# Kernel optimization log

Measured on AMD Instinct MI355X. Metric: run time of the kernel, lower is better.

Reference implementation:

```python
import jax, jax.numpy as jnp
import numpy as np
from jax import lax

DIM, HEADS, POOL = 512, 8, 16
HD = DIM // HEADS
SCALE = HD ** -0.5


def _cbs(x, w, s, b, d=1, g=1):
    """Conv2d(bias=False, pad=d*(k-1)//2) + folded BN (scale,bias) + SiLU."""
    k = w.shape[-1]
    p = d * (k - 1) // 2
    y = lax.conv_general_dilated(x, w, (1, 1), [(p, p), (p, p)],
                                 rhs_dilation=(d, d), feature_group_count=g,
                                 dimension_numbers=("NCHW", "OIHW", "NCHW"))
    y = y * s[None, :, None, None] + b[None, :, None, None]
    return y * jax.nn.sigmoid(y)  # SiLU


def _forward(x, w01, s01, b01, w02, s02, b02, w03, s03, b03,
             w12, s12, b12, w13, s13, b13, w22, s22, b22, w23, s23, b23,
             w3, s3, b3, wkv, skv, bkv, wfc1, bfc1, wfc2, bfc2):
    bsz, c, h, w = x.shape
    # ---- _MutilScal ----
    a01 = _cbs(x, w01, s01, b01)                       # [b,128,h,w]
    a03 = _cbs(_cbs(a01, w02, s02, b02, d=3, g=128), w03, s03, b03)
    a13 = _cbs(_cbs(a01, w12, s12, b12, d=5, g=128), w13, s13, b13)
    a23 = _cbs(_cbs(a01, w22, s22, b22, d=7, g=128), w23, s23, b23)
    attn = _cbs(a03 + a13 + a23, w3, s3, b3) * x       # [b,512,h,w]
    # AdaptiveAvgPool2d(POOL): exact block mean since h,w divisible by POOL
    pooled = attn.reshape(bsz, c, POOL, h // POOL, POOL, w // POOL).mean(axis=(3, 5))
    kv = _cbs(pooled, wkv, skv, bkv)                   # [b,1024,16,16]
    # ---- pooled cross-attention ----
    n, n1 = h * w, POOL * POOL
    q = x.reshape(bsz, HEADS, HD, n).transpose(0, 1, 3, 2)          # [b,H,n,d]
    kvr = kv.reshape(bsz, 2, HEADS, HD, n1)
    k = kvr[:, 0].transpose(0, 1, 3, 2)                              # [b,H,n1,d]
    v = kvr[:, 1].transpose(0, 1, 3, 2)                              # [b,H,n1,d]
    dots = jnp.einsum("bhnd,bhmd->bhnm", q, k) * SCALE
    a = jax.nn.softmax(dots, axis=-1)
    o = jnp.einsum("bhnm,bhmd->bhnd", a, v)                          # [b,H,n,d]
    attn_out = o.transpose(0, 1, 3, 2).reshape(bsz, c, h, w)
    # ---- SE channel gate ----
    gap = x.mean(axis=(2, 3))                                        # [b,c]
    y = jnp.clip(gap @ wfc1[:, :, 0, 0].T + bfc1, 0.0, 6.0)          # ReLU6
    gate = jax.nn.sigmoid(y @ wfc2[:, :, 0, 0].T + bfc2)             # [b,c]
    c_attn = gate[:, :, None, None] * x
    return attn_out + c_attn


def setup_inputs() -> dict:
    key = jax.random.key(0)
    ks = jax.random.split(key, 32)
    ki = iter(ks)
    f = jnp.float32

    def rn(shape, scale=0.05):
        return (jax.random.normal(next(ki), shape, dtype=f) * scale)

    inp = {"x": jax.random.normal(next(ki), (8, DIM, 64, 64), dtype=f)}
    inp.update(w01=rn((128, 512, 1, 1)), s01=jnp.ones((128,), f), b01=rn((128,)))
    inp.update(w02=rn((128, 1, 3, 3)), s02=jnp.ones((128,), f), b02=rn((128,)))
    inp.update(w03=rn((512, 128, 1, 1)), s03=jnp.ones((512,), f), b03=rn((512,)))
    inp.update(w12=rn((128, 1, 3, 3)), s12=jnp.ones((128,), f), b12=rn((128,)))
    inp.update(w13=rn((512, 128, 1, 1)), s13=jnp.ones((512,), f), b13=rn((512,)))
    inp.update(w22=rn((128, 1, 3, 3)), s22=jnp.ones((128,), f), b22=rn((128,)))
    inp.update(w23=rn((512, 128, 1, 1)), s23=jnp.ones((512,), f), b23=rn((512,)))
    inp.update(w3=rn((512, 512, 1, 1)), s3=jnp.ones((512,), f), b3=rn((512,)))
    inp.update(wkv=rn((1024, 512, 1, 1)), skv=jnp.ones((1024,), f), bkv=rn((1024,)))
    inp.update(wfc1=rn((128, 512, 1, 1)), bfc1=rn((128,)))
    inp.update(wfc2=rn((512, 128, 1, 1)), bfc2=rn((512,)))
    return inp


def reference(x, w01, s01, b01, w02, s02, b02, w03, s03, b03,
              w12, s12, b12, w13, s13, b13, w22, s22, b22, w23, s23, b23,
              w3, s3, b3, wkv, skv, bkv, wfc1, bfc1, wfc2, bfc2):
    return _forward(x, w01, s01, b01, w02, s02, b02, w03, s03, b03,
                    w12, s12, b12, w13, s13, b13, w22, s22, b22, w23, s23, b23,
                    w3, s3, b3, wkv, skv, bkv, wfc1, bfc1, wfc2, bfc2)
```

## Files before the change

### kernel.cpp

```cpp
#include <hip/hip_runtime.h>
#include <cstddef>


static __device__ __forceinline__ float silu_f(float v) {
  return v / (1.f + __expf(-v));
}

typedef __attribute__((ext_vector_type(8))) short short8v;
typedef __attribute__((ext_vector_type(4))) float f32x4;

union FragU { unsigned u[4]; short8v v; uint4 q; };

#define VM_WAIT(N) asm volatile("s_waitcnt vmcnt(" #N ")" ::: "memory")
#define SBAR()     asm volatile("s_barrier" ::: "memory")

static __device__ __forceinline__ unsigned short f2bf(float f) {
  unsigned u = __builtin_bit_cast(unsigned, f);
  u += 0x7fffu + ((u >> 16) & 1u);
  return (unsigned short)(u >> 16);
}
static __device__ __forceinline__ unsigned packbf(float lo, float hi) {
  return (unsigned)f2bf(lo) | ((unsigned)f2bf(hi) << 16);
}
static __device__ __forceinline__ float bf_lo(unsigned w) {
  return __builtin_bit_cast(float, w << 16);
}
static __device__ __forceinline__ float bf_hi(unsigned w) {
  return __builtin_bit_cast(float, w & 0xffff0000u);
}

static __device__ __forceinline__ void gload16(const unsigned* gsrc, unsigned* ldst) {
  __builtin_amdgcn_global_load_lds(
      (const __attribute__((address_space(1))) unsigned*)gsrc,
      (__attribute__((address_space(3))) unsigned*)ldst, 16, 0, 0);
}

static __device__ __forceinline__ void stage_tile_g(const unsigned* __restrict__ src,
                                                    unsigned* dst, int tid) {
  gload16(src + 4 * tid, dst + 4 * tid);
  gload16(src + 4 * (tid + 512), dst + 4 * (tid + 512));
}

static __device__ __forceinline__ short8v load_frag4(const unsigned* P, int ksg, int pos) {
  FragU f;
  f.q = *(const uint4*)(P + (((ksg << 7) + pos) << 2));
  return f.v;
}

static __device__ __forceinline__ void xload16(const float* __restrict__ src, int ld,
                                               int tid, float v[16]) {
  const int pos = tid & 127, kg = tid >> 7;
  const float* p = src + pos + (size_t)(kg * 16) * ld;
#pragma unroll
  for (int i = 0; i < 16; ++i) v[i] = p[(size_t)i * ld];
}
static __device__ __forceinline__ void xload16_sum2(const float* __restrict__ a,
                                                    const float* __restrict__ b2, int ld,
                                                    int tid, float v[16]) {
  const int pos = tid & 127, kg = tid >> 7;
  const float* pA = a + pos + (size_t)(kg * 16) * ld;
  const float* pB = b2 + pos + (size_t)(kg * 16) * ld;
#pragma unroll
  for (int i = 0; i < 16; ++i) v[i] = pA[(size_t)i * ld] + pB[(size_t)i * ld];
}
static __device__ __forceinline__ void xwrite16(const float v[16], unsigned* Xp, int tid) {
  const int pos = tid & 127, kg = tid >> 7;
#pragma unroll
  for (int i2 = 0; i2 < 4; ++i2) {
    const int kq = kg * 4 + i2;
    const int r4 = (kq & 3) + ((kq >> 3) << 2);
    const int sub = (kq >> 2) & 1;
    uint2 wv;
    wv.x = packbf(v[i2 * 4 + 0], v[i2 * 4 + 1]);
    wv.y = packbf(v[i2 * 4 + 2], v[i2 * 4 + 3]);
    *(uint2*)(Xp + (((r4 << 7) + pos) << 2) + sub * 2) = wv;
  }
}
static __device__ __forceinline__ void xstore_pairs(const float v[16],
                                                    unsigned* __restrict__ Xg_bst,
                                                    int p0, int tid) {
  const int pos = tid & 127, kg = tid >> 7;
#pragma unroll
  for (int m = 0; m < 8; ++m)
    Xg_bst[(size_t)(kg * 8 + m) * 4096 + p0 + pos] = packbf(v[2 * m], v[2 * m + 1]);
}

static __device__ __forceinline__ void stage_x_pack(const float* __restrict__ src, int ld,
                                                    unsigned* Xp, int tid) {
  float v[16];
  xload16(src, ld, tid, v);
  xwrite16(v, Xp, tid);
}

#define GEMM_IDS                                            \
  const int tid = threadIdx.x;                              \
  const int w = tid >> 6, lane = tid & 63;                  \
  const int g = lane >> 4, nl = lane & 15;                  \
  const int wr = w >> 1, wc = w & 1;

#define GEMM_KSTEP_B(ACC, XB, WB)                                                  \
  _Pragma("unroll")                                                                \
  for (int ks = 0; ks < 2; ++ks) {                                                 \
    const short8v a0 = load_frag4(WB, ks * 4 + g, wr * 32 + nl);                   \
    const short8v a1 = load_frag4(WB, ks * 4 + g, wr * 32 + 16 + nl);              \
    _Pragma("unroll")                                                              \
    for (int jj = 0; jj < 4; ++jj) {                                               \
      const short8v bfr = load_frag4(XB, ks * 4 + g, wc * 64 + jj * 16 + nl);      \
      ACC[0][jj] = __builtin_amdgcn_mfma_f32_16x16x32_bf16(a0, bfr, ACC[0][jj], 0, 0, 0); \
      ACC[1][jj] = __builtin_amdgcn_mfma_f32_16x16x32_bf16(a1, bfr, ACC[1][jj], 0, 0, 0); \
    }                                                                              \
  }

__global__ __launch_bounds__(256)
void prepack_w_kernel(const float* __restrict__ w01, const float* __restrict__ w03,
                      const float* __restrict__ w13, const float* __restrict__ w23,
                      const float* __restrict__ w3, const float* __restrict__ wkv,
                      unsigned* __restrict__ img)
{
  const int t = blockIdx.x;
  const float* W; int K; int tile; unsigned* base;
  if (t < 8)       { W = w01; K = 512; tile = t;      base = img; }
  else if (t < 16) { W = w03; K = 128; tile = t - 8;  base = img + 32768; }
  else if (t < 24) { W = w13; K = 128; tile = t - 16; base = img + 65536; }
  else if (t < 32) { W = w23; K = 128; tile = t - 24; base = img + 98304; }
  else if (t < 64) { W = w3;  K = 512; tile = t - 32; base = img + 131072; }
  else             { W = wkv; K = 512; tile = t - 64; base = img + 262144; }
  const int nk = K >> 6;
  const int to = tile / nk, tk = tile - to * nk;
  unsigned* dst = base + (size_t)tile * 4096;
  for (int wi = threadIdx.x; wi < 4096; wi += 256) {
    const int r4 = wi >> 9, pos = (wi >> 2) & 127, sub = (wi >> 1) & 1, j = wi & 1;
    const int kq = (r4 & 3) + sub * 4 + ((r4 >> 2) << 3);
    const int k = tk * 64 + 4 * kq + 2 * j;
    const int oc = to * 128 + pos;
    dst[wi] = packbf(W[(size_t)oc * K + k], W[(size_t)oc * K + k + 1]);
  }
}

__global__ __launch_bounds__(512)
void gemm_a01_kernel(const float* __restrict__ X, const unsigned* __restrict__ Wimg,
                     const float* __restrict__ sc, const float* __restrict__ bi,
                     unsigned* __restrict__ A01p, unsigned* __restrict__ Ximg2)
{
  const int b = blockIdx.z, p0 = blockIdx.x * 128;
  GEMM_IDS
  __shared__ unsigned Xp[2][4096], Wp[2][4096];
  const float* Xbase = X + (size_t)b * 512 * 4096 + p0;
  unsigned* Xg_b = Ximg2 + (size_t)b * 256 * 4096;

  f32x4 acc[2][4];
#pragma unroll
  for (int i = 0; i < 2; ++i)
#pragma unroll
    for (int jj = 0; jj < 4; ++jj) acc[i][jj] = (f32x4){0.f, 0.f, 0.f, 0.f};

  {
    float vx[16];
    xload16(Xbase, 4096, tid, vx);
    stage_tile_g(Wimg, Wp[0], tid);
    xwrite16(vx, Xp[0], tid);
    xstore_pairs(vx, Xg_b, p0, tid);
  }
  __syncthreads();

  for (int st = 0; st < 8; ++st) {
    const int cur = st & 1;
    float vn[16];
    if (st < 7) {
      xload16(Xbase + (size_t)((st + 1) * 64) * 4096, 4096, tid, vn);
      stage_tile_g(Wimg + (size_t)(st + 1) * 4096, Wp[cur ^ 1], tid);
    }
    GEMM_KSTEP_B(acc, Xp[cur], Wp[cur])
    if (st < 7) {
      xwrite16(vn, Xp[cur ^ 1], tid);
      xstore_pairs(vn, Xg_b + (size_t)(32 * (st + 1)) * 4096, p0, tid);
    }
    __syncthreads();
  }

#pragma unroll
  for (int i = 0; i < 2; ++i) {
    const int base = wr * 32 + i * 16 + 4 * g;
    const float s0_ = sc[base + 0], b0_ = bi[base + 0];
    const float s1_ = sc[base + 1], b1_ = bi[base + 1];
    const float s2_ = sc[base + 2], b2_ = bi[base + 2];
    const float s3_ = sc[base + 3], b3_ = bi[base + 3];
#pragma unroll
    for (int jj = 0; jj < 4; ++jj) {
      const int pos = p0 + wc * 64 + jj * 16 + nl;
      const float v0 = silu_f(s0_ * acc[i][jj][0] + b0_);
      const float v1 = silu_f(s1_ * acc[i][jj][1] + b1_);
      const float v2 = silu_f(s2_ * acc[i][jj][2] + b2_);
      const float v3 = silu_f(s3_ * acc[i][jj][3] + b3_);
      A01p[((size_t)b * 64 + (base >> 1)) * 4096 + pos]     = packbf(v0, v1);
      A01p[((size_t)b * 64 + (base >> 1) + 1) * 4096 + pos] = packbf(v2, v3);
    }
  }
}

__global__ __launch_bounds__(256)
void dwconv_pack_kernel(const unsigned* __restrict__ A01p, unsigned* __restrict__ Timg,
                        const float* __restrict__ w02, const float* __restrict__ s02, const float* __restrict__ b02,
                        const float* __restrict__ w12, const float* __restrict__ s12, const float* __restrict__ b12,
                        const float* __restrict__ w22, const float* __restrict__ s22, const float* __restrict__ b22)
{
  const int br = blockIdx.z;
  const int yb = blockIdx.y;
  const int b = yb >> 4, t16 = yb & 15, kstep = t16 >> 3, mm = t16 & 7;
  const int kq = (mm & 3) + ((mm >> 2) << 3);
  const int cbase = kstep * 64 + kq * 4;
  const int p = blockIdx.x * 256 + threadIdx.x;
  const int y = p >> 6, xx = p & 63;
  const int d = 3 + 2 * br;

  const float* wsel = br == 0 ? w02 : (br == 1 ? w12 : w22);
  const float* ssel = br == 0 ? s02 : (br == 1 ? s12 : s22);
  const float* bsel = br == 0 ? b02 : (br == 1 ? b12 : b22);

  float sum[8] = {};
  const unsigned* plane0 = A01p + ((size_t)b * 64 + (cbase >> 1)) * 4096;

#pragma unroll
  for (int u = -1; u <= 1; ++u) {
    const int yv = y + u * d;
    if ((unsigned)yv < 64u) {
#pragma unroll
      for (int v = -1; v <= 1; ++v) {
        const int xv = xx + v * d;
        if ((unsigned)xv < 64u) {
          const int idx = yv * 64 + xv;
          const int tap = (u + 1) * 3 + (v + 1);
#pragma unroll
          for (int q = 0; q < 4; ++q) {
            const int sub = q >> 1, jw = q & 1;
            const unsigned wv = plane0[(size_t)(sub * 8 + jw) * 4096 + idx];
            const int ch = cbase + sub * 16 + jw * 2;
            sum[q * 2 + 0] += wsel[(ch + 0) * 9 + tap] * bf_lo(wv);
            sum[q * 2 + 1] += wsel[(ch + 1) * 9 + tap] * bf_hi(wv);
          }
        }
      }
    }
  }

  unsigned wout[4];
#pragma unroll
  for (int h = 0; h < 4; ++h) {
    const int ch = cbase + (h >> 1) * 16 + (h & 1) * 2;
    const float va = silu_f(ssel[ch] * sum[h * 2] + bsel[ch]);
    const float vb = silu_f(ssel[ch + 1] * sum[h * 2 + 1] + bsel[ch + 1]);
    wout[h] = packbf(va, vb);
  }
  const int tile = ((br * 8 + b) * 2 + kstep) * 32 + (p >> 7);
  *(uint4*)(Timg + (size_t)tile * 4096 + (((mm << 7) + (p & 127)) << 2)) = *(uint4*)wout;
}

__global__ __launch_bounds__(512)
void gemm3branch_img_kernel(const unsigned* __restrict__ Timg, const unsigned* __restrict__ Wimg3,
                            const float* __restrict__ s0, const float* __restrict__ s1, const float* __restrict__ s2,
                            const float* __restrict__ b0, const float* __restrict__ b1, const float* __restrict__ b2,
                            unsigned* __restrict__ Bimg)
{
  const int b = blockIdx.z, pt = blockIdx.x, oc0 = blockIdx.y * 128;
  GEMM_IDS
  __shared__ unsigned Xp[2][4096], Wp[2][4096];

  float sum[2][4][4] = {};
  f32x4 acc[2][4];
#pragma unroll
  for (int i = 0; i < 2; ++i)
#pragma unroll
    for (int jj = 0; jj < 4; ++jj) acc[i][jj] = (f32x4){0.f, 0.f, 0.f, 0.f};

#define SRC_X3(st) (Timg + (((size_t)(((st) >> 1) * 8 + b) * 2 + ((st) & 1)) * 32 + pt) * 4096)
#define SRC_W3(st) (Wimg3 + (size_t)((st) >> 1) * 32768 + ((size_t)(oc0 >> 7) * 2 + ((st) & 1)) * 4096)

  stage_tile_g(SRC_X3(0), Xp[0], tid);
  stage_tile_g(SRC_W3(0), Wp[0], tid);
  __syncthreads();

  for (int st = 0; st < 6; ++st) {
    const int cur = st & 1;
    if (st < 5) {
      stage_tile_g(SRC_X3(st + 1), Xp[cur ^ 1], tid);
      stage_tile_g(SRC_W3(st + 1), Wp[cur ^ 1], tid);
    }
    GEMM_KSTEP_B(acc, Xp[cur], Wp[cur])
    if (st & 1) {
      const int brn = st >> 1;
      const float* ss = brn == 0 ? s0 : (brn == 1 ? s1 : s2);
      const float* bs = brn == 0 ? b0 : (brn == 1 ? b1 : b2);
#pragma unroll
      for (int i = 0; i < 2; ++i) {
        const int base = oc0 + wr * 32 + i * 16 + 4 * g;
#pragma unroll
        for (int r = 0; r < 4; ++r) {
          const float s = ss[base + r], bb = bs[base + r];
#pragma unroll
          for (int jj = 0; jj < 4; ++jj) {
            sum[i][jj][r] += silu_f(s * acc[i][jj][r] + bb);
            acc[i][jj][r] = 0.f;
          }
        }
      }
    }
    __syncthreads();
  }
#undef SRC_X3
#undef SRC_W3

#pragma unroll
  for (int i = 0; i < 2; ++i) {
    const int ol = wr * 32 + i * 16 + 4 * g;
    const int kstep_g = (oc0 + ol) >> 6;
    const int kin = ol & 63;
    const int kq2 = kin >> 2;
    const int r4 = (kq2 & 3) + ((kq2 >> 3) << 2);
    const int sub = (kq2 >> 2) & 1;
#pragma unroll
    for (int jj = 0; jj < 4; ++jj) {
      const int pos = wc * 64 + jj * 16 + nl;
      uint2 wv;
      wv.x = packbf(sum[i][jj][0], sum[i][jj][1]);
      wv.y = packbf(sum[i][jj][2], sum[i][jj][3]);
      *(uint2*)(Bimg + ((size_t)(b * 8 + kstep_g) * 32 + pt) * 4096 + (((r4 << 7) + pos) << 2) + sub * 2) = wv;
    }
  }
}

__global__ __launch_bounds__(512)
void gemm_pool_img_kernel(const unsigned* __restrict__ Bimg, const unsigned* __restrict__ W3img,
                          const float* __restrict__ sc, const float* __restrict__ bi,
                          const unsigned* __restrict__ Ximg2, float* __restrict__ pooled2,
                          float* __restrict__ gapb)
{
  const int b = blockIdx.z, pt = blockIdx.x, oc0 = blockIdx.y * 128;
  const int p0 = pt * 128;
  const unsigned* Xb2 = Ximg2 + (size_t)b * 256 * 4096;
  GEMM_IDS
  __shared__ unsigned Xp[2][4096], Wp[2][4096];

  f32x4 acc[2][4];
#pragma unroll
  for (int i = 0; i < 2; ++i)
#pragma unroll
    for (int jj = 0; jj < 4; ++jj) acc[i][jj] = (f32x4){0.f, 0.f, 0.f, 0.f};

#define SRC_XP(st) (Bimg + ((size_t)(b * 8 + (st)) * 32 + pt) * 4096)
#define SRC_WP(st) (W3img + ((size_t)(oc0 >> 7) * 8 + (st)) * 4096)

  stage_tile_g(SRC_XP(0), Xp[0], tid);
  stage_tile_g(SRC_WP(0), Wp[0], tid);
  stage_tile_g(SRC_XP(1), Xp[1], tid);
  stage_tile_g(SRC_WP(1), Wp[1], tid);

#pragma unroll
  for (int st = 0; st < 8; ++st) {
    const int cur = st & 1;
    if (st < 7) { VM_WAIT(4); } else { VM_WAIT(0); }
    SBAR();
    __builtin_amdgcn_s_setprio(1);
    GEMM_KSTEP_B(acc, Xp[cur], Wp[cur])
    __builtin_amdgcn_s_setprio(0);
    SBAR();
    if (st < 6) {
      stage_tile_g(SRC_XP(st + 2), Xp[cur], tid);
      stage_tile_g(SRC_WP(st + 2), Wp[cur], tid);
    }
  }
#undef SRC_XP
#undef SRC_WP

  float* red  = (float*)Wp[0];
  float* gred = red + 2048;
  for (int e = tid; e < 2176; e += 512) red[e] = 0.f;
  __syncthreads();

  float xsum[2][4] = {};
#pragma unroll
  for (int i = 0; i < 2; ++i) {
    const int olb = wr * 32 + i * 16 + 4 * g;
    const int oc_ = oc0 + olb;
    const float4 s4 = *(const float4*)(sc + oc_);
    const float4 b4 = *(const float4*)(bi + oc_);
#pragma unroll
    for (int jj = 0; jj < 4; ++jj) {
      const int p = p0 + wc * 64 + jj * 16 + nl;
      const unsigned xw0 = Xb2[(size_t)(oc_ >> 1) * 4096 + p];
      const unsigned xw1 = Xb2[(size_t)((oc_ >> 1) + 1) * 4096 + p];
      const float xv[4] = {bf_lo(xw0), bf_hi(xw0), bf_lo(xw1), bf_hi(xw1)};
      const float sv[4] = {s4.x, s4.y, s4.z, s4.w};
      const float bv[4] = {b4.x, b4.y, b4.z, b4.w};
#pragma unroll
      for (int r = 0; r < 4; ++r) {
        xsum[i][r] += xv[r];
        float val = silu_f(sv[r] * acc[i][jj][r] + bv[r]) * xv[r];
        val += __shfl_xor(val, 1, 64);
        val += __shfl_xor(val, 2, 64);
        if ((nl & 3) == 0) {
          const int col = p & 63;
          atomicAdd(&red[(olb + r) * 16 + (col >> 2)], val);
        }
      }
    }
  }
#pragma unroll
  for (int i = 0; i < 2; ++i)
#pragma unroll
    for (int r = 0; r < 4; ++r) {
      float v = xsum[i][r];
      v += __shfl_xor(v, 1, 64);
      v += __shfl_xor(v, 2, 64);
      v += __shfl_xor(v, 4, 64);
      v += __shfl_xor(v, 8, 64);
      if (nl == 0)
        atomicAdd(&gred[wr * 32 + i * 16 + 4 * g + r], v);
    }
  __syncthreads();

  {
    const int ph = pt >> 1;
    float* pdst = pooled2 + (size_t)(pt & 1) * (8ull * 512 * 256);
    for (int e = tid; e < 2048; e += 512) {
      const int ol = e >> 4, pw = e & 15;
      pdst[((size_t)b * 512 + oc0 + ol) * 256 + ph * 16 + pw] = red[e] * (1.f / 16.f);
    }
    if (tid < 128)
      atomicAdd(&gapb[b * 512 + oc0 + tid], gred[tid]);
  }
}

__global__ __launch_bounds__(512)
void gemm_kv_kernel(const float* __restrict__ pooled2, const unsigned* __restrict__ WKVimg,
                    const float* __restrict__ sc, const float* __restrict__ bi,
                    unsigned* __restrict__ Kimg, unsigned* __restrict__ Vimg)
{
  const int b = blockIdx.z, p0 = blockIdx.x * 128, oc0 = blockIdx.y * 128;
  const float* XbA = pooled2 + (size_t)b * 512 * 256 + p0;
  const float* XbB = XbA + 8ull * 512 * 256;
  GEMM_IDS
  __shared__ unsigned Xp[2][4096], Wp[2][4096];

  f32x4 acc[2][4];
#pragma unroll
  for (int i = 0; i < 2; ++i)
#pragma unroll
    for (int jj = 0; jj < 4; ++jj) acc[i][jj] = (f32x4){0.f, 0.f, 0.f, 0.f};

  {
    float vx[16];
    xload16_sum2(XbA, XbB, 256, tid, vx);
    stage_tile_g(WKVimg + (size_t)(oc0 >> 7) * 8 * 4096, Wp[0], tid);
    xwrite16(vx, Xp[0], tid);
  }
  __syncthreads();

  for (int st = 0; st < 8; ++st) {
    const int cur = st & 1;
    float vn[16];
    if (st < 7) {
      xload16_sum2(XbA + (size_t)((st + 1) * 64) * 256, XbB + (size_t)((st + 1) * 64) * 256,
                   256, tid, vn);
      stage_tile_g(WKVimg + ((size_t)(oc0 >> 7) * 8 + st + 1) * 4096, Wp[cur ^ 1], tid);
    }
    GEMM_KSTEP_B(acc, Xp[cur], Wp[cur])
    if (st < 7) xwrite16(vn, Xp[cur ^ 1], tid);
    __syncthreads();
  }

  const bool isK = (oc0 < 512);
#pragma unroll
  for (int i = 0; i < 2; ++i) {
    const int ocb = oc0 + wr * 32 + i * 16 + 4 * g;
#pragma unroll
    for (int jj = 0; jj < 4; ++jj) {
      const int pos = p0 + wc * 64 + jj * 16 + nl;
      float v[4];
#pragma unroll
      for (int r = 0; r < 4; ++r)
        v[r] = silu_f(sc[ocb + r] * acc[i][jj][r] + bi[ocb + r]);
      const int ch = pos >> 7, ml = pos & 127;
      if (isK) {
        const int h = ocb >> 6, d0 = ocb & 63;
        const int kq = d0 >> 2, sub = (kq >> 2) & 1;
        const int r4 = (kq & 3) + ((kq >> 3) << 2);
        unsigned* t = Kimg + ((size_t)(b * 8 + h) * 2 + ch) * 4096;
        uint2 wv;
        wv.x = packbf(v[0] * 0.125f, v[1] * 0.125f);
        wv.y = packbf(v[2] * 0.125f, v[3] * 0.125f);
        *(uint2*)(t + (((r4 << 7) + ml) << 2) + sub * 2) = wv;
      } else {
        const int h = (ocb - 512) >> 6, d0 = (ocb - 512) & 63;
        unsigned* t = Vimg + ((size_t)(b * 8 + h) * 2 + ch) * 4096;
        float ov[4];
#pragma unroll
        for (int r = 0; r < 4; ++r) ov[r] = __shfl_xor(v[r], 1, 64);
        if ((nl & 1) == 0) {
          const int s = (ml >> 1) & 1, m4 = ml >> 2;
#pragma unroll
          for (int r = 0; r < 4; ++r)
            t[((m4 * 64 + d0 + r) << 1) + s] = packbf(v[r], ov[r]);
        }
      }
    }
  }
}

__global__ __launch_bounds__(512)
void se_kernel(const float* __restrict__ gap,
               const float* __restrict__ wfc1, const float* __restrict__ bfc1,
               const float* __restrict__ wfc2, const float* __restrict__ bfc2,
               float* __restrict__ gate)
{
  const int b = blockIdx.x, tid = threadIdx.x;
  __shared__ float ylds[128];
  if (tid < 128) {
    float a = 0.f;
    for (int c = 0; c < 512; ++c) a += gap[b * 512 + c] * wfc1[tid * 512 + c];
    a = a * (1.f / 4096.f) + bfc1[tid];
    ylds[tid] = fminf(fmaxf(a, 0.f), 6.f);
  }
  __syncthreads();
  float g = 0.f;
  for (int j = 0; j < 128; ++j) g += ylds[j] * wfc2[tid * 128 + j];
  g += bfc2[tid];
  gate[b * 512 + tid] = 1.f / (1.f + __expf(-g));
}

__global__ __launch_bounds__(512)
void attn_mfma_kernel(const float* __restrict__ x, const unsigned* __restrict__ Kimg,
                      const unsigned* __restrict__ Vimg,
                      const float* __restrict__ gate, float* __restrict__ out)
{
  const int b = blockIdx.z, h = blockIdx.y;
  const int n0 = blockIdx.x * 128;
  const int tid = threadIdx.x;
  const int w = tid >> 6, lane = tid & 63;
  const int g = lane >> 4, nl = lane & 15;

  __shared__ unsigned lds[20480];
  unsigned* Qp = lds;
  unsigned* Kb0 = lds + 4096;
  unsigned* Kb1 = lds + 8192;
  unsigned* Vb0 = lds + 12288;
  unsigned* Vb1 = lds + 16384;
  float* Osm = (float*)(lds + 4096);

  const size_t tbase = (size_t)(b * 8 + h) * 2 * 4096;

  stage_tile_g(Kimg + tbase, Kb0, tid);
  stage_tile_g(Vimg + tbase, Vb0, tid);
  stage_x_pack(x + ((size_t)b * 512 + h * 64) * 4096 + n0, 4096, Qp, tid);
  __syncthreads();
  stage_tile_g(Kimg + tbase + 4096, Kb1, tid);
  stage_tile_g(Vimg + tbase + 4096, Vb1, tid);

  float m_run = -1e30f, l_run = 0.f;
  f32x4 o[4];
#pragma unroll
  for (int i = 0; i < 4; ++i) o[i] = (f32x4){0.f, 0.f, 0.f, 0.f};

#pragma unroll
  for (int ch = 0; ch < 2; ++ch) {
    const unsigned* Kp = ch ? Kb1 : Kb0;
    const unsigned* Vp = ch ? Vb1 : Vb0;

    f32x4 s[8];
#pragma unroll
    for (int mb = 0; mb < 8; ++mb) s[mb] = (f32x4){0.f, 0.f, 0.f, 0.f};
#pragma unroll
    for (int ks = 0; ks < 2; ++ks) {
      const short8v qf = load_frag4(Qp, ks * 4 + g, w * 16 + nl);
#pragma unroll
      for (int mb = 0; mb < 8; ++mb) {
        const short8v kf = load_frag4(Kp, ks * 4 + g, mb * 16 + nl);
        s[mb] = __builtin_amdgcn_mfma_f32_16x16x32_bf16(kf, qf, s[mb], 0, 0, 0);
      }
    }

    float cm = -1e30f;
#pragma unroll
    for (int mb = 0; mb < 8; ++mb)
#pragma unroll
      for (int r = 0; r < 4; ++r) cm = fmaxf(cm, s[mb][r]);
    cm = fmaxf(cm, __shfl_xor(cm, 16, 64));
    cm = fmaxf(cm, __shfl_xor(cm, 32, 64));
    const float mnew = fmaxf(m_run, cm);
    const float corr = __expf(m_run - mnew);
    m_run = mnew;
    float cs = 0.f;
#pragma unroll
    for (int mb = 0; mb < 8; ++mb)
#pragma unroll
      for (int r = 0; r < 4; ++r) {
        const float p = __expf(s[mb][r] - mnew);
        s[mb][r] = p;
        cs += p;
      }
    cs += __shfl_xor(cs, 16, 64);
    cs += __shfl_xor(cs, 32, 64);
    l_run = l_run * corr + cs;
#pragma unroll
    for (int db = 0; db < 4; ++db)
#pragma unroll
      for (int r = 0; r < 4; ++r) o[db][r] *= corr;

#pragma unroll
    for (int ks = 0; ks < 4; ++ks) {
      FragU pf;
      pf.u[0] = packbf(s[2 * ks][0],     s[2 * ks][1]);
      pf.u[1] = packbf(s[2 * ks][2],     s[2 * ks][3]);
      pf.u[2] = packbf(s[2 * ks + 1][0], s[2 * ks + 1][1]);
      pf.u[3] = packbf(s[2 * ks + 1][2], s[2 * ks + 1][3]);
#pragma unroll
      for (int db = 0; db < 4; ++db) {
        FragU vf;
        const uint2 lo = *(const uint2*)(Vp + ((8 * ks + g) * 64 + db * 16 + nl) * 2);
        const uint2 hi = *(const uint2*)(Vp + ((8 * ks + 4 + g) * 64 + db * 16 + nl) * 2);
        vf.u[0] = lo.x; vf.u[1] = lo.y; vf.u[2] = hi.x; vf.u[3] = hi.y;
        o[db] = __builtin_amdgcn_mfma_f32_16x16x32_bf16(vf.v, pf.v, o[db], 0, 0, 0);
      }
    }
    __syncthreads();
  }

  const float inv = 1.f / l_run;
#pragma unroll
  for (int db = 0; db < 4; ++db)
#pragma unroll
    for (int r = 0; r < 4; ++r)
      Osm[(db * 16 + 4 * g + r) * 132 + w * 16 + nl] = o[db][r] * inv;
  __syncthreads();

  {
    const int n = tid & 127, t7 = tid >> 7;
    const int jw = t7 >> 1, half = t7 & 1;
#pragma unroll
    for (int i = 0; i < 16; ++i) {
      const int d = t7 + 4 * i;
      const int r4 = (i & 3) + ((i >> 3) << 2);
      const int sub = (i >> 2) & 1;
      const unsigned xw = Qp[(((r4 << 7) + n) << 2) + sub * 2 + jw];
      const float xv = half ? bf_hi(xw) : bf_lo(xw);
      const int c2 = h * 64 + d;
      const size_t off = ((size_t)b * 512 + c2) * 4096 + n0 + n;
      out[off] = Osm[d * 132 + n] + gate[b * 512 + c2] * xv;
    }
  }
}

extern "C" void kernel_launch(void* const* d_in, const int* in_sizes, int n_in,
                              void* d_out, int out_size, void* d_ws, size_t ws_size,
                              hipStream_t stream)
{
  const float* x    = (const float*)d_in[0];
  const float* w01  = (const float*)d_in[1];
  const float* s01  = (const float*)d_in[2];
  const float* b01  = (const float*)d_in[3];
  const float* w02  = (const float*)d_in[4];
  const float* s02  = (const float*)d_in[5];
  const float* b02  = (const float*)d_in[6];
  const float* w03  = (const float*)d_in[7];
  const float* s03  = (const float*)d_in[8];
  const float* b03  = (const float*)d_in[9];
  const float* w12  = (const float*)d_in[10];
  const float* s12  = (const float*)d_in[11];
  const float* b12  = (const float*)d_in[12];
  const float* w13  = (const float*)d_in[13];
  const float* s13  = (const float*)d_in[14];
  const float* b13  = (const float*)d_in[15];
  const float* w22  = (const float*)d_in[16];
  const float* s22  = (const float*)d_in[17];
  const float* b22  = (const float*)d_in[18];
  const float* w23  = (const float*)d_in[19];
  const float* s23  = (const float*)d_in[20];
  const float* b23  = (const float*)d_in[21];
  const float* w3   = (const float*)d_in[22];
  const float* s3   = (const float*)d_in[23];
  const float* b3   = (const float*)d_in[24];
  const float* wkv  = (const float*)d_in[25];
  const float* skv  = (const float*)d_in[26];
  const float* bkv  = (const float*)d_in[27];
  const float* wfc1 = (const float*)d_in[28];
  const float* bfc1 = (const float*)d_in[29];
  const float* wfc2 = (const float*)d_in[30];
  const float* bfc2 = (const float*)d_in[31];

  float* out = (float*)d_out;
  unsigned* wsu = (unsigned*)d_ws;

  unsigned* Timg    = wsu;
  float*    pooled2 = (float*)(wsu + 6291456);
  unsigned* Kimg    = wsu + 8388608;
  unsigned* Vimg    = wsu + 8912896;
  float*    gapb    = (float*)(wsu + 9437184);
  float*    gateb   = (float*)(wsu + 9441280);
  unsigned* Wimg    = wsu + 9445376;

  unsigned* A01p  = (unsigned*)d_out;
  unsigned* Bimg  = (unsigned*)d_out;
  unsigned* Ximg2 = (unsigned*)d_out + 8388608;

  prepack_w_kernel<<<128, 256, 0, stream>>>(w01, w03, w13, w23, w3, wkv, Wimg);
  gemm_a01_kernel<<<dim3(32, 1, 8), 512, 0, stream>>>(x, Wimg, s01, b01, A01p, Ximg2);
  dwconv_pack_kernel<<<dim3(16, 128, 3), 256, 0, stream>>>(A01p, Timg,
      w02, s02, b02, w12, s12, b12, w22, s22, b22);
  gemm3branch_img_kernel<<<dim3(32, 4, 8), 512, 0, stream>>>(Timg, Wimg + 32768,
      s03, s13, s23, b03, b13, b23, Bimg);
  hipMemsetAsync(gapb, 0, 4096 * sizeof(float), stream);
  gemm_pool_img_kernel<<<dim3(32, 4, 8), 512, 0, stream>>>(Bimg, Wimg + 131072,
      s3, b3, Ximg2, pooled2, gapb);
  gemm_kv_kernel<<<dim3(2, 8, 8), 512, 0, stream>>>(pooled2, Wimg + 262144, skv, bkv, Kimg, Vimg);
  se_kernel<<<8, 512, 0, stream>>>(gapb, wfc1, bfc1, wfc2, bfc2, gateb);
  attn_mfma_kernel<<<dim3(32, 8, 8), 512, 0, stream>>>(x, Kimg, Vimg, gateb, out);
}
```

Measured before the change: 233.2 us.

## Rewrite pool GEMM with 256 threads, single LDS buffer, larger per-wave tiles

```diff
diff --git a/kernel.cpp b/kernel.cpp
--- a/kernel.cpp
+++ b/kernel.cpp
@@ -10,9 +10,6 @@
 typedef __attribute__((ext_vector_type(4))) float f32x4;
 
 union FragU { unsigned u[4]; short8v v; uint4 q; };
-
-#define VM_WAIT(N) asm volatile("s_waitcnt vmcnt(" #N ")" ::: "memory")
-#define SBAR()     asm volatile("s_barrier" ::: "memory")
 
 static __device__ __forceinline__ unsigned short f2bf(float f) {
   unsigned u = __builtin_bit_cast(unsigned, f);
@@ -39,6 +36,13 @@
                                                     unsigned* dst, int tid) {
   gload16(src + 4 * tid, dst + 4 * tid);
   gload16(src + 4 * (tid + 512), dst + 4 * (tid + 512));
+}
+
+static __device__ __forceinline__ void stage_tile_g256(const unsigned* __restrict__ src,
+                                                       unsigned* dst, int tid) {
+#pragma unroll
+  for (int k = 0; k < 4; ++k)
+    gload16(src + k * 1024 + tid * 4, dst + k * 1024 + tid * 4);
 }
 
 static __device__ __forceinline__ short8v load_frag4(const unsigned* P, int ksg, int pos) {
@@ -328,7 +332,7 @@
   }
 }
 
-__global__ __launch_bounds__(512)
+__global__ __launch_bounds__(256)
 void gemm_pool_img_kernel(const unsigned* __restrict__ Bimg, const unsigned* __restrict__ W3img,
                           const float* __restrict__ sc, const float* __restrict__ bi,
                           const unsigned* __restrict__ Ximg2, float* __restrict__ pooled2,
@@ -337,49 +341,50 @@
   const int b = blockIdx.z, pt = blockIdx.x, oc0 = blockIdx.y * 128;
   const int p0 = pt * 128;
   const unsigned* Xb2 = Ximg2 + (size_t)b * 256 * 4096;
-  GEMM_IDS
-  __shared__ unsigned Xp[2][4096], Wp[2][4096];
-
-  f32x4 acc[2][4];
-#pragma unroll
-  for (int i = 0; i < 2; ++i)
+  const int tid = threadIdx.x;
+  const int w = tid >> 6, lane = tid & 63;
+  const int g = lane >> 4, nl = lane & 15;
+  const int wr = w >> 1, wc = w & 1;
+
+  __shared__ unsigned Xp[4096], Wp[4096];
+
+  f32x4 acc[4][4];
+#pragma unroll
+  for (int i = 0; i < 4; ++i)
 #pragma unroll
     for (int jj = 0; jj < 4; ++jj) acc[i][jj] = (f32x4){0.f, 0.f, 0.f, 0.f};
 
-#define SRC_XP(st) (Bimg + ((size_t)(b * 8 + (st)) * 32 + pt) * 4096)
-#define SRC_WP(st) (W3img + ((size_t)(oc0 >> 7) * 8 + (st)) * 4096)
-
-  stage_tile_g(SRC_XP(0), Xp[0], tid);
-  stage_tile_g(SRC_WP(0), Wp[0], tid);
-  stage_tile_g(SRC_XP(1), Xp[1], tid);
-  stage_tile_g(SRC_WP(1), Wp[1], tid);
-
-#pragma unroll
   for (int st = 0; st < 8; ++st) {
-    const int cur = st & 1;
-    if (st < 7) { VM_WAIT(4); } else { VM_WAIT(0); }
-    SBAR();
-    __builtin_amdgcn_s_setprio(1);
-    GEMM_KSTEP_B(acc, Xp[cur], Wp[cur])
-    __builtin_amdgcn_s_setprio(0);
-    SBAR();
-    if (st < 6) {
-      stage_tile_g(SRC_XP(st + 2), Xp[cur], tid);
-      stage_tile_g(SRC_WP(st + 2), Wp[cur], tid);
-    }
-  }
-#undef SRC_XP
-#undef SRC_WP
-
-  float* red  = (float*)Wp[0];
+    __syncthreads();
+    stage_tile_g256(Bimg + ((size_t)(b * 8 + st) * 32 + pt) * 4096, Xp, tid);
+    stage_tile_g256(W3img + ((size_t)(oc0 >> 7) * 8 + st) * 4096, Wp, tid);
+    __syncthreads();
+#pragma unroll
+    for (int ks = 0; ks < 2; ++ks) {
+      short8v a[4];
+#pragma unroll
+      for (int i = 0; i < 4; ++i)
+        a[i] = load_frag4(Wp, ks * 4 + g, wr * 64 + i * 16 + nl);
+#pragma unroll
+      for (int jj = 0; jj < 4; ++jj) {
+        const short8v bfr = load_frag4(Xp, ks * 4 + g, wc * 64 + jj * 16 + nl);
+#pragma unroll
+        for (int i = 0; i < 4; ++i)
+          acc[i][jj] = __builtin_amdgcn_mfma_f32_16x16x32_bf16(a[i], bfr, acc[i][jj], 0, 0, 0);
+      }
+    }
+  }
+  __syncthreads();
+
+  float* red  = (float*)Wp;
   float* gred = red + 2048;
-  for (int e = tid; e < 2176; e += 512) red[e] = 0.f;
-  __syncthreads();
-
-  float xsum[2][4] = {};
-#pragma unroll
-  for (int i = 0; i < 2; ++i) {
-    const int olb = wr * 32 + i * 16 + 4 * g;
+  for (int e = tid; e < 2176; e += 256) red[e] = 0.f;
+  __syncthreads();
+
+  float xsum[4][4] = {};
+#pragma unroll
+  for (int i = 0; i < 4; ++i) {
+    const int olb = wr * 64 + i * 16 + 4 * g;
     const int oc_ = oc0 + olb;
     const float4 s4 = *(const float4*)(sc + oc_);
     const float4 b4 = *(const float4*)(bi + oc_);
@@ -405,7 +410,7 @@
     }
   }
 #pragma unroll
-  for (int i = 0; i < 2; ++i)
+  for (int i = 0; i < 4; ++i)
 #pragma unroll
     for (int r = 0; r < 4; ++r) {
       float v = xsum[i][r];
@@ -414,14 +419,14 @@
       v += __shfl_xor(v, 4, 64);
       v += __shfl_xor(v, 8, 64);
       if (nl == 0)
-        atomicAdd(&gred[wr * 32 + i * 16 + 4 * g + r], v);
+        atomicAdd(&gred[wr * 64 + i * 16 + 4 * g + r], v);
     }
   __syncthreads();
 
   {
     const int ph = pt >> 1;
     float* pdst = pooled2 + (size_t)(pt & 1) * (8ull * 512 * 256);
-    for (int e = tid; e < 2048; e += 512) {
+    for (int e = tid; e < 2048; e += 256) {
       const int ol = e >> 4, pw = e & 15;
       pdst[((size_t)b * 512 + oc0 + ol) * 256 + ph * 16 + pw] = red[e] * (1.f / 16.f);
     }
@@ -708,7 +713,7 @@
   gemm3branch_img_kernel<<<dim3(32, 4, 8), 512, 0, stream>>>(Timg, Wimg + 32768,
       s03, s13, s23, b03, b13, b23, Bimg);
   hipMemsetAsync(gapb, 0, 4096 * sizeof(float), stream);
-  gemm_pool_img_kernel<<<dim3(32, 4, 8), 512, 0, stream>>>(Bimg, Wimg + 131072,
+  gemm_pool_img_kernel<<<dim3(32, 4, 8), 256, 0, stream>>>(Bimg, Wimg + 131072,
       s3, b3, Ximg2, pooled2, gapb);
   gemm_kv_kernel<<<dim3(2, 8, 8), 512, 0, stream>>>(pooled2, Wimg + 262144, skv, bkv, Kimg, Vimg);
   se_kernel<<<8, 512, 0, stream>>>(gapb, wfc1, bfc1, wfc2, bfc2, gateb);
```

Result: slower. 239.5 us (+2.7%).
